# Kernel tuning notes

Hardware: AMD Instinct MI355X
Metric: run time of the kernel (lower is better)

The kernel has to match this reference:

```python
import jax, jax.numpy as jnp
import numpy as np

NEG_SLOPE = 0.2  # PyG GATConv default


def leaky_relu(v):
    return jnp.where(v >= 0, v, NEG_SLOPE * v)


def gat_conv(x, W, a_src, a_dst, b, src, dst, n_nodes):
    # x: [N, Fin], W: [Fin, Fout], a_src/a_dst/b: [Fout]
    h = x @ W                               # [N, Fout]
    alpha_src = h @ a_src                   # [N]
    alpha_dst = h @ a_dst                   # [N]
    e = leaky_relu(alpha_src[src] + alpha_dst[dst])          # [E]
    m = jax.ops.segment_max(e, dst, num_segments=n_nodes)    # [N] (self-loops => every node has >=1 edge)
    p = jnp.exp(e - m[dst])                                   # [E]
    s = jax.ops.segment_sum(p, dst, num_segments=n_nodes)     # [N]
    coef = p / s[dst]                                          # [E]
    out = jax.ops.segment_sum(coef[:, None] * h[src], dst, num_segments=n_nodes)
    return out + b


def setup_inputs() -> dict:
    key = jax.random.key(0)
    ks = jax.random.split(key, 20)
    N, E, DIN, DH, DOUT, G = 50000, 800000, 128, 256, 2, 512
    x = jax.random.normal(ks[0], (N, DIN), dtype=jnp.float32)
    edge_index = jax.random.randint(ks[1], (2, E), 0, N, dtype=jnp.int64)
    batch = jnp.sort(jax.random.randint(ks[2], (N,), 0, G, dtype=jnp.int64))

    def lin(k, fin, fout):
        return jax.random.normal(k, (fin, fout), dtype=jnp.float32) * (1.0 / np.sqrt(fin))

    def att(k, f):
        return jax.random.normal(k, (f,), dtype=jnp.float32) * (1.0 / np.sqrt(f))

    return {
        "x": x, "edge_index": edge_index, "batch": batch,
        "W1": lin(ks[3], DIN, DH), "as1": att(ks[4], DH), "ad1": att(ks[5], DH), "b1": jnp.zeros((DH,), jnp.float32),
        "W2": lin(ks[6], DH, DH),  "as2": att(ks[7], DH), "ad2": att(ks[8], DH), "b2": jnp.zeros((DH,), jnp.float32),
        "W3": lin(ks[9], DH, DH),  "as3": att(ks[10], DH), "ad3": att(ks[11], DH), "b3": jnp.zeros((DH,), jnp.float32),
        "Wfc": lin(ks[12], DH, DOUT), "bfc": jnp.zeros((DOUT,), jnp.float32),
    }


def reference(x, edge_index, batch, W1, as1, ad1, b1, W2, as2, ad2, b2, W3, as3, ad3, b3, Wfc, bfc):
    N = x.shape[0]
    G = 512  # number of graphs (static)
    # add self-loops (PyG GATConv default add_self_loops=True)
    loops = jnp.arange(N, dtype=edge_index.dtype)
    src = jnp.concatenate([edge_index[0], loops])
    dst = jnp.concatenate([edge_index[1], loops])

    h = jax.nn.relu(gat_conv(x, W1, as1, ad1, b1, src, dst, N))
    h = jax.nn.relu(gat_conv(h, W2, as2, ad2, b2, src, dst, N))
    h = jax.nn.relu(gat_conv(h, W3, as3, ad3, b3, src, dst, N))

    # global mean pool over graphs
    sums = jax.ops.segment_sum(h, batch, num_segments=G)                 # [G, DH]
    counts = jax.ops.segment_sum(jnp.ones((N,), h.dtype), batch, num_segments=G)
    pooled = sums / jnp.maximum(counts, 1.0)[:, None]

    logits = pooled @ Wfc + bfc                                           # [G, DOUT]
    return jax.nn.softmax(logits, axis=1)
```

## Files before the change

kernel.cpp:

```cpp
#include <hip/hip_runtime.h>
#include <hip/hip_bf16.h>

typedef short short8 __attribute__((ext_vector_type(8)));
typedef float floatx4 __attribute__((ext_vector_type(4)));
typedef unsigned short ushort_t;
typedef unsigned short ushort4v __attribute__((ext_vector_type(4)));

__device__ __forceinline__ ushort_t f2bf(float v) {
    __hip_bfloat16 h = __float2bfloat16(v);
    return *(ushort_t*)&h;
}
__device__ __forceinline__ float bf2f(ushort_t u) {
    return __uint_as_float(((unsigned)u) << 16);
}
__device__ __forceinline__ float4 ldh4(const ushort_t* p) {
    ushort4v u = *(const ushort4v*)p;
    return make_float4(bf2f(u.x), bf2f(u.y), bf2f(u.z), bf2f(u.w));
}


__device__ __forceinline__ void wsplit_store(const float* __restrict__ W, int K,
                                             ushort_t* __restrict__ Bthi,
                                             ushort_t* __restrict__ Btlo,
                                             int idx, bool permK) {
    int n = idx & 255, k = idx >> 8;
    int i = k & 63;
    int ko = permK ? ((k & ~63) | ((i & 3) << 4) | (i >> 2)) : k;
    float v = W[(size_t)ko * 256 + n];
    ushort_t h = f2bf(v);
    float r = v - bf2f(h);
    int nt = n >> 4, c = k >> 5, q = (k & 31) >> 3, j = k & 7;
    int l = q * 16 + (n & 15);
    size_t off = ((size_t)(nt * (K >> 5) + c) * 64 + l) * 8 + j;
    Bthi[off] = h;
    Btlo[off] = f2bf(r);
}

__global__ __launch_bounds__(256) void prep_kernel(const float* __restrict__ X,
                                                   ushort_t* __restrict__ Xhi,
                                                   ushort_t* __restrict__ Xlo,
                                                   int* __restrict__ deg,
                                                   float* __restrict__ asrcA,
                                                   float* __restrict__ adstA,
                                                   const float* __restrict__ W1,
                                                   const float* __restrict__ W2,
                                                   const float* __restrict__ W3,
                                                   ushort_t* __restrict__ B1h, ushort_t* __restrict__ B1l,
                                                   ushort_t* __restrict__ B2h, ushort_t* __restrict__ B2l,
                                                   ushort_t* __restrict__ B3h, ushort_t* __restrict__ B3l,
                                                   int total, int N) {
    int idx = blockIdx.x * 256 + threadIdx.x;
    if (idx < N) {
        deg[idx] = 0;
        asrcA[idx] = 0.f;
        adstA[idx] = 0.f;
    }
    const int S1 = 128 * 256, S2 = 256 * 256;
    if (idx < S1) {
        wsplit_store(W1, 128, B1h, B1l, idx, false);
    } else if (idx < S1 + S2) {
        wsplit_store(W2, 256, B2h, B2l, idx - S1, true);
    } else if (idx < S1 + 2 * S2) {
        wsplit_store(W3, 256, B3h, B3l, idx - S1 - S2, true);
    }
    if (idx < total) {
        float v = X[idx];
        ushort_t h = f2bf(v);
        Xhi[idx] = h;
        Xlo[idx] = f2bf(v - bf2f(h));
    }
}

template <int NCHUNK, bool HASLO>
__global__ __launch_bounds__(256) void gemm_mfma(const ushort_t* __restrict__ Ahi_g,
                                                 const ushort_t* __restrict__ Alo_g,
                                                 const ushort_t* __restrict__ Bthi,
                                                 const ushort_t* __restrict__ Btlo,
                                                 ushort_t* __restrict__ Hb,
                                                 const float* __restrict__ a_src,
                                                 const float* __restrict__ a_dst,
                                                 float* __restrict__ asrc_out,
                                                 float* __restrict__ adst_out,
                                                 int N) {
    constexpr int K = NCHUNK * 32;
    const int tid = threadIdx.x;
    const int wave = tid >> 6, lane = tid & 63;
    const int wr = wave & 1, wc = wave >> 1;
    const int q = lane >> 4, l15 = lane & 15;
    const int rowBase = blockIdx.x * 128;
    const int colBase = blockIdx.y * 128;

    floatx4 acc[4][4];
#pragma unroll
    for (int i = 0; i < 4; ++i)
#pragma unroll
        for (int j = 0; j < 4; ++j) acc[i][j] = (floatx4)0.f;

    size_t aoff[4];
#pragma unroll
    for (int mt = 0; mt < 4; ++mt) {
        int r = rowBase + wr * 64 + mt * 16 + l15;
        if (r > N - 1) r = N - 1;
        aoff[mt] = (size_t)r * K + q * 8;
    }

    const int ntg = blockIdx.y * 8 + wc * 4;
    const size_t ntstride = (size_t)NCHUNK * 512;
    const ushort_t* bhp = Bthi + (size_t)ntg * ntstride + (size_t)lane * 8;
    const ushort_t* blp = Btlo + (size_t)ntg * ntstride + (size_t)lane * 8;

#pragma unroll
    for (int c = 0; c < NCHUNK; ++c) {
        const int co = c * 32;
        const size_t cb = (size_t)c * 512;
        short8 ah[4], al[4], bh[4], bl[4];
#pragma unroll
        for (int mt = 0; mt < 4; ++mt)
            ah[mt] = *(const short8*)(Ahi_g + aoff[mt] + co);
        if (HASLO) {
#pragma unroll
            for (int mt = 0; mt < 4; ++mt)
                al[mt] = *(const short8*)(Alo_g + aoff[mt] + co);
        }
#pragma unroll
        for (int nt = 0; nt < 4; ++nt) {
            bh[nt] = *(const short8*)(bhp + (size_t)nt * ntstride + cb);
            bl[nt] = *(const short8*)(blp + (size_t)nt * ntstride + cb);
        }
#pragma unroll
        for (int mt = 0; mt < 4; ++mt)
#pragma unroll
            for (int nt = 0; nt < 4; ++nt) {
                acc[mt][nt] = __builtin_amdgcn_mfma_f32_16x16x32_bf16(ah[mt], bh[nt], acc[mt][nt], 0, 0, 0);
                acc[mt][nt] = __builtin_amdgcn_mfma_f32_16x16x32_bf16(ah[mt], bl[nt], acc[mt][nt], 0, 0, 0);
            }
        if (HASLO) {
#pragma unroll
            for (int mt = 0; mt < 4; ++mt)
#pragma unroll
                for (int nt = 0; nt < 4; ++nt)
                    acc[mt][nt] = __builtin_amdgcn_mfma_f32_16x16x32_bf16(al[mt], bh[nt], acc[mt][nt], 0, 0, 0);
        }
    }

    float asv[4], adv[4];
#pragma unroll
    for (int nt = 0; nt < 4; ++nt) {
        int n = colBase + wc * 64 + nt * 16 + l15;
        asv[nt] = a_src[n];
        adv[nt] = a_dst[n];
    }
#pragma unroll
    for (int mt = 0; mt < 4; ++mt) {
#pragma unroll
        for (int reg = 0; reg < 4; ++reg) {
            int grow = rowBase + wr * 64 + mt * 16 + q * 4 + reg;
            float p1 = acc[mt][0][reg] * asv[0] + acc[mt][1][reg] * asv[1] +
                       acc[mt][2][reg] * asv[2] + acc[mt][3][reg] * asv[3];
            float p2 = acc[mt][0][reg] * adv[0] + acc[mt][1][reg] * adv[1] +
                       acc[mt][2][reg] * adv[2] + acc[mt][3][reg] * adv[3];
            if (grow < N) {
                uint2 pk;
                pk.x = (unsigned)f2bf(acc[mt][0][reg]) | ((unsigned)f2bf(acc[mt][1][reg]) << 16);
                pk.y = (unsigned)f2bf(acc[mt][2][reg]) | ((unsigned)f2bf(acc[mt][3][reg]) << 16);
                *(uint2*)(Hb + (size_t)grow * 256 + colBase + wc * 64 + l15 * 4) = pk;
            }
#pragma unroll
            for (int off = 1; off < 16; off <<= 1) {
                p1 += __shfl_xor(p1, off, 64);
                p2 += __shfl_xor(p2, off, 64);
            }
            if (l15 == 0 && grow < N) {
                atomicAdd(&asrc_out[grow], p1);
                atomicAdd(&adst_out[grow], p2);
            }
        }
    }
}

__global__ __launch_bounds__(256) void count_kernel(const int* __restrict__ edst,
                                                    int* __restrict__ deg, int E) {
    int i = blockIdx.x * 256 + threadIdx.x;
    if (i < E) atomicAdd(&deg[edst[i]], 1);
}

__global__ __launch_bounds__(256) void scan1_kernel(const int* __restrict__ deg,
                                                    int* __restrict__ excl,
                                                    int* __restrict__ bsum, int N) {
    __shared__ int tmp[256];
    int tid = threadIdx.x;
    int i = blockIdx.x * 256 + tid;
    int v = (i < N) ? deg[i] : 0;
    tmp[tid] = v;
    __syncthreads();
    for (int off = 1; off < 256; off <<= 1) {
        int t = (tid >= off) ? tmp[tid - off] : 0;
        __syncthreads();
        tmp[tid] += t;
        __syncthreads();
    }
    if (i < N) excl[i] = tmp[tid] - v;
    if (tid == 255) bsum[blockIdx.x] = tmp[255];
}

__global__ __launch_bounds__(256) void scan2_kernel(int* __restrict__ bsum, int nb) {
    __shared__ int tmp[256];
    int tid = threadIdx.x;
    int v = (tid < nb) ? bsum[tid] : 0;
    tmp[tid] = v;
    __syncthreads();
    for (int off = 1; off < 256; off <<= 1) {
        int t = (tid >= off) ? tmp[tid - off] : 0;
        __syncthreads();
        tmp[tid] += t;
        __syncthreads();
    }
    if (tid < nb) bsum[tid] = tmp[tid] - v;
}

__global__ __launch_bounds__(256) void scan3_kernel(const int* __restrict__ excl,
                                                    const int* __restrict__ bsum,
                                                    int* __restrict__ rowptr,
                                                    int* __restrict__ cursor,
                                                    int N, int E) {
    int i = blockIdx.x * 256 + threadIdx.x;
    if (i < N) {
        int v = excl[i] + bsum[blockIdx.x];
        rowptr[i] = v;
        cursor[i] = v;
    }
    if (i == 0) rowptr[N] = E;
}

__global__ __launch_bounds__(256) void scatter_kernel(const int* __restrict__ esrc,
                                                      const int* __restrict__ edst,
                                                      int* __restrict__ cursor,
                                                      int* __restrict__ csr_src, int E) {
    int i = blockIdx.x * 256 + threadIdx.x;
    if (i < E) {
        int d = edst[i];
        int pos = atomicAdd(&cursor[d], 1);
        csr_src[pos] = esrc[i];
    }
}

__global__ __launch_bounds__(256) void gat_fused_kernel(const ushort_t* __restrict__ hb,
                                                        const float* __restrict__ asrc,
                                                        const float* __restrict__ adst,
                                                        const int* __restrict__ rowptr,
                                                        const int* __restrict__ csr_src,
                                                        const float* __restrict__ bias,
                                                        ushort_t* __restrict__ ohi,
                                                        float* __restrict__ asrc_next,
                                                        float* __restrict__ adst_next,
                                                        int N) {
    int wave = threadIdx.x >> 6;
    int lane = threadIdx.x & 63;
    int d = blockIdx.x * 4 + wave;
    if (d >= N) return;

    if (lane == 0) {
        asrc_next[d] = 0.f;
        adst_next[d] = 0.f;
    }

    const float* bb = bias + (lane >> 4) * 64 + (lane & 15);
    float b0 = bb[0], b1 = bb[16], b2 = bb[32], b3 = bb[48];

    float ad = adst[d];
    float es = asrc[d] + ad;
    es = es >= 0.f ? es : 0.2f * es;
    float m = es;
    float s = 1.0f;
    float4 acc = ldh4(hb + (size_t)d * 256 + lane * 4);

    int beg = rowptr[d], end = rowptr[d + 1];
    for (int base = beg; base < end; base += 64) {
        int cnt = min(64, end - base);
        int srci = 0;
        float e = -1e30f;
        if (lane < cnt) {
            srci = csr_src[base + lane];
            float v = asrc[srci] + ad;
            e = v >= 0.f ? v : 0.2f * v;
        }
        float cm = e;
#pragma unroll
        for (int off = 32; off > 0; off >>= 1) cm = fmaxf(cm, __shfl_xor(cm, off, 64));
        float mnew = fmaxf(m, cm);
        float scale = __expf(m - mnew);
        m = mnew;

        float p = __expf(e - m);
        float ps = p;
#pragma unroll
        for (int off = 32; off > 0; off >>= 1) ps += __shfl_xor(ps, off, 64);
        s = s * scale + ps;
        acc.x *= scale; acc.y *= scale; acc.z *= scale; acc.w *= scale;

        int j = 0;
        for (; j + 4 <= cnt; j += 4) {
            float p0 = __shfl(p, j, 64),     p1 = __shfl(p, j + 1, 64);
            float p2 = __shfl(p, j + 2, 64), p3 = __shfl(p, j + 3, 64);
            int s0 = __shfl(srci, j, 64),     s1i = __shfl(srci, j + 1, 64);
            int s2i = __shfl(srci, j + 2, 64), s3i = __shfl(srci, j + 3, 64);
            float4 hv0 = ldh4(hb + (size_t)s0 * 256 + lane * 4);
            float4 hv1 = ldh4(hb + (size_t)s1i * 256 + lane * 4);
            float4 hv2 = ldh4(hb + (size_t)s2i * 256 + lane * 4);
            float4 hv3 = ldh4(hb + (size_t)s3i * 256 + lane * 4);
            acc.x += p0 * hv0.x + p1 * hv1.x + p2 * hv2.x + p3 * hv3.x;
            acc.y += p0 * hv0.y + p1 * hv1.y + p2 * hv2.y + p3 * hv3.y;
            acc.z += p0 * hv0.z + p1 * hv1.z + p2 * hv2.z + p3 * hv3.z;
            acc.w += p0 * hv0.w + p1 * hv1.w + p2 * hv2.w + p3 * hv3.w;
        }
        for (; j < cnt; ++j) {
            float pj = __shfl(p, j, 64);
            int sj = __shfl(srci, j, 64);
            float4 hv = ldh4(hb + (size_t)sj * 256 + lane * 4);
            acc.x += pj * hv.x; acc.y += pj * hv.y; acc.z += pj * hv.z; acc.w += pj * hv.w;
        }
    }
    float inv = 1.0f / s;
    float ox = fmaxf(acc.x * inv + b0, 0.f);
    float oy = fmaxf(acc.y * inv + b1, 0.f);
    float oz = fmaxf(acc.z * inv + b2, 0.f);
    float ow = fmaxf(acc.w * inv + b3, 0.f);
    ushort4v hv;
    hv.x = f2bf(ox); hv.y = f2bf(oy); hv.z = f2bf(oz); hv.w = f2bf(ow);
    *(ushort4v*)(ohi + (size_t)d * 256 + lane * 4) = hv;
}

__device__ __forceinline__ int lower_bound_i(const int* __restrict__ a, int n, int v) {
    int lo = 0, hi = n;
    while (lo < hi) {
        int mid = (lo + hi) >> 1;
        if (a[mid] < v) lo = mid + 1; else hi = mid;
    }
    return lo;
}

__global__ __launch_bounds__(256) void pool_fc_kernel(const ushort_t* __restrict__ hhi,
                                                      const int* __restrict__ batch,
                                                      int N,
                                                      const float* __restrict__ Wfc,
                                                      const float* __restrict__ bfc,
                                                      float* __restrict__ out) {
    __shared__ float red0[256];
    __shared__ float red1[256];
    int g = blockIdx.x;
    int c = threadIdx.x;
    int i = c & 63;
    int o = (c & ~63) | ((i & 3) << 4) | (i >> 2);
    int beg = lower_bound_i(batch, N, g);
    int end = lower_bound_i(batch, N, g + 1);
    float sum = 0.f;
    for (int n = beg; n < end; ++n)
        sum += bf2f(hhi[(size_t)n * 256 + c]);
    float cnt = (float)(end - beg);
    float v = sum / fmaxf(cnt, 1.0f);
    red0[c] = v * Wfc[o * 2 + 0];
    red1[c] = v * Wfc[o * 2 + 1];
    __syncthreads();
    for (int off = 128; off > 0; off >>= 1) {
        if (c < off) {
            red0[c] += red0[c + off];
            red1[c] += red1[c + off];
        }
        __syncthreads();
    }
    if (c == 0) {
        float l0 = red0[0] + bfc[0];
        float l1 = red1[0] + bfc[1];
        float mx = fmaxf(l0, l1);
        float e0 = expf(l0 - mx), e1 = expf(l1 - mx);
        float s = e0 + e1;
        out[g * 2 + 0] = e0 / s;
        out[g * 2 + 1] = e1 / s;
    }
}

extern "C" void kernel_launch(void* const* d_in, const int* in_sizes, int n_in,
                              void* d_out, int out_size, void* d_ws, size_t ws_size,
                              hipStream_t stream) {
    const float* x    = (const float*)d_in[0];
    const int*   eidx = (const int*)d_in[1];
    const int*   batch= (const int*)d_in[2];
    const float* Wl[3]  = {(const float*)d_in[3], (const float*)d_in[7],  (const float*)d_in[11]};
    const float* asl[3] = {(const float*)d_in[4], (const float*)d_in[8],  (const float*)d_in[12]};
    const float* adl[3] = {(const float*)d_in[5], (const float*)d_in[9],  (const float*)d_in[13]};
    const float* bl[3]  = {(const float*)d_in[6], (const float*)d_in[10], (const float*)d_in[14]};
    const float* Wfc = (const float*)d_in[15];
    const float* bfc = (const float*)d_in[16];
    float* out = (float*)d_out;

    const int N   = in_sizes[2];
    const int E   = in_sizes[1] / 2;
    const int DIN = in_sizes[0] / N;
    const int DH  = 256;
    const int G   = 512;
    const int* esrc = eidx;
    const int* edst = eidx + E;

    char* ws = (char*)d_ws;
    size_t off = 0;
    const size_t featHalf = (size_t)N * DH * sizeof(ushort_t);
    ushort_t* hb     = (ushort_t*)(ws + off); off += featHalf;
    ushort_t* ghi    = (ushort_t*)(ws + off); off += featHalf;
    ushort_t* xhi    = (ushort_t*)(ws + off); off += (size_t)N * DIN * sizeof(ushort_t);
    ushort_t* xlo    = (ushort_t*)(ws + off); off += (size_t)N * DIN * sizeof(ushort_t);
    float*    asA    = (float*)(ws + off); off += (size_t)N * sizeof(float);
    float*    adA    = (float*)(ws + off); off += (size_t)N * sizeof(float);
    float*    asB    = (float*)(ws + off); off += (size_t)N * sizeof(float);
    float*    adB    = (float*)(ws + off); off += (size_t)N * sizeof(float);
    int*      deg    = (int*)(ws + off);   off += (size_t)N * sizeof(int);
    int*      excl   = (int*)(ws + off);   off += (size_t)N * sizeof(int);
    int*      rowptr = (int*)(ws + off);   off += (size_t)(N + 1) * sizeof(int);
    int*      cursor = (int*)(ws + off);   off += (size_t)N * sizeof(int);
    int*      bsum   = (int*)(ws + off);   off += 1024;
    int*      csrsrc = (int*)(ws + off);   off += (size_t)E * sizeof(int);
    ushort_t* B1h    = (ushort_t*)(ws + off); off += (size_t)128 * 256 * sizeof(ushort_t);
    ushort_t* B1l    = (ushort_t*)(ws + off); off += (size_t)128 * 256 * sizeof(ushort_t);
    ushort_t* B2h    = (ushort_t*)(ws + off); off += (size_t)256 * 256 * sizeof(ushort_t);
    ushort_t* B2l    = (ushort_t*)(ws + off); off += (size_t)256 * 256 * sizeof(ushort_t);
    ushort_t* B3h    = (ushort_t*)(ws + off); off += (size_t)256 * 256 * sizeof(ushort_t);
    ushort_t* B3l    = (ushort_t*)(ws + off); off += (size_t)256 * 256 * sizeof(ushort_t);

    const int nbN = (N + 255) / 256;

    prep_kernel<<<((size_t)N * DIN + 255) / 256, 256, 0, stream>>>(
        x, xhi, xlo, deg, asA, adA, Wl[0], Wl[1], Wl[2],
        B1h, B1l, B2h, B2l, B3h, B3l, N * DIN, N);

    count_kernel<<<(E + 255) / 256, 256, 0, stream>>>(edst, deg, E);
    scan1_kernel<<<nbN, 256, 0, stream>>>(deg, excl, bsum, N);
    scan2_kernel<<<1, 256, 0, stream>>>(bsum, nbN);
    scan3_kernel<<<nbN, 256, 0, stream>>>(excl, bsum, rowptr, cursor, N, E);
    scatter_kernel<<<(E + 255) / 256, 256, 0, stream>>>(esrc, edst, cursor, csrsrc, E);

    const ushort_t* Bh[3]  = {B1h, B2h, B3h};
    const ushort_t* Blp[3] = {B1l, B2l, B3l};
    float* asCur[3] = {asA, asB, asA};
    float* adCur[3] = {adA, adB, adA};
    float* asNext[3] = {asB, asA, asB};
    float* adNext[3] = {adB, adA, adB};

    dim3 ggrid((N + 127) / 128, 2);
    for (int layer = 0; layer < 3; ++layer) {
        if (layer == 0) {
            gemm_mfma<4, true><<<ggrid, 256, 0, stream>>>(xhi, xlo, Bh[0], Blp[0], hb,
                                                          asl[0], adl[0], asCur[0], adCur[0], N);
        } else {
            gemm_mfma<8, false><<<ggrid, 256, 0, stream>>>(ghi, nullptr, Bh[layer], Blp[layer], hb,
                                                           asl[layer], adl[layer],
                                                           asCur[layer], adCur[layer], N);
        }

        gat_fused_kernel<<<(N + 3) / 4, 256, 0, stream>>>(hb, asCur[layer], adCur[layer],
                                                          rowptr, csrsrc, bl[layer], ghi,
                                                          asNext[layer], adNext[layer], N);
    }

    pool_fc_kernel<<<G, 256, 0, stream>>>(ghi, batch, N, Wfc, bfc, out);
}
```

Measured before the change: 517.9 us.

## Give each GEMM wave full-width rows so attention scores need no atomics

The GEMM now launches one block per 128 rows instead of splitting columns across two blocks. Each wave computes 32 rows by all 256 columns, so the per-row attention dot products are complete inside the wave and are written with plain stores instead of atomicAdd. This removes the score zeroing in prep and gat kernels and the ping-pong buffers. The weight split in prep now writes coalesced. The trade-off is 128 accumulator registers per wave, which may lower occupancy, and B tiles are no longer reused across the wave's row tiles in the same way.

After: 610.4 us. 17.9% more time.

```diff
diff --git a/kernel.cpp b/kernel.cpp
--- a/kernel.cpp
+++ b/kernel.cpp
@@ -19,29 +19,30 @@
 }
 
 
-__device__ __forceinline__ void wsplit_store(const float* __restrict__ W, int K,
-                                             ushort_t* __restrict__ Bthi,
-                                             ushort_t* __restrict__ Btlo,
-                                             int idx, bool permK) {
-    int n = idx & 255, k = idx >> 8;
-    int i = k & 63;
-    int ko = permK ? ((k & ~63) | ((i & 3) << 4) | (i >> 2)) : k;
+template <int NCSHIFT>
+__device__ __forceinline__ void wsplit_coal(const float* __restrict__ W,
+                                            ushort_t* __restrict__ Bh,
+                                            ushort_t* __restrict__ Bl,
+                                            int o, bool permK) {
+    int j = o & 7;
+    int l = (o >> 3) & 63;
+    int rest = o >> 9;
+    int nt = rest >> NCSHIFT;
+    int c  = rest & ((1 << NCSHIFT) - 1);
+    int n  = nt * 16 + (l & 15);
+    int ks = c * 32 + (l >> 4) * 8 + j;
+    int i = ks & 63;
+    int ko = permK ? ((ks & ~63) | ((i & 3) << 4) | (i >> 2)) : ks;
     float v = W[(size_t)ko * 256 + n];
     ushort_t h = f2bf(v);
-    float r = v - bf2f(h);
-    int nt = n >> 4, c = k >> 5, q = (k & 31) >> 3, j = k & 7;
-    int l = q * 16 + (n & 15);
-    size_t off = ((size_t)(nt * (K >> 5) + c) * 64 + l) * 8 + j;
-    Bthi[off] = h;
-    Btlo[off] = f2bf(r);
+    Bh[o] = h;
+    Bl[o] = f2bf(v - bf2f(h));
 }
 
 __global__ __launch_bounds__(256) void prep_kernel(const float* __restrict__ X,
                                                    ushort_t* __restrict__ Xhi,
                                                    ushort_t* __restrict__ Xlo,
                                                    int* __restrict__ deg,
-                                                   float* __restrict__ asrcA,
-                                                   float* __restrict__ adstA,
                                                    const float* __restrict__ W1,
                                                    const float* __restrict__ W2,
                                                    const float* __restrict__ W3,
@@ -50,18 +51,14 @@
                                                    ushort_t* __restrict__ B3h, ushort_t* __restrict__ B3l,
                                                    int total, int N) {
     int idx = blockIdx.x * 256 + threadIdx.x;
-    if (idx < N) {
-        deg[idx] = 0;
-        asrcA[idx] = 0.f;
-        adstA[idx] = 0.f;
-    }
+    if (idx < N) deg[idx] = 0;
     const int S1 = 128 * 256, S2 = 256 * 256;
     if (idx < S1) {
-        wsplit_store(W1, 128, B1h, B1l, idx, false);
+        wsplit_coal<2>(W1, B1h, B1l, idx, false);
     } else if (idx < S1 + S2) {
-        wsplit_store(W2, 256, B2h, B2l, idx - S1, true);
+        wsplit_coal<3>(W2, B2h, B2l, idx - S1, true);
     } else if (idx < S1 + 2 * S2) {
-        wsplit_store(W3, 256, B3h, B3l, idx - S1 - S2, true);
+        wsplit_coal<3>(W3, B3h, B3l, idx - S1 - S2, true);
     }
     if (idx < total) {
         float v = X[idx];
@@ -85,85 +82,84 @@
     constexpr int K = NCHUNK * 32;
     const int tid = threadIdx.x;
     const int wave = tid >> 6, lane = tid & 63;
-    const int wr = wave & 1, wc = wave >> 1;
     const int q = lane >> 4, l15 = lane & 15;
-    const int rowBase = blockIdx.x * 128;
-    const int colBase = blockIdx.y * 128;
-
-    floatx4 acc[4][4];
-#pragma unroll
-    for (int i = 0; i < 4; ++i)
-#pragma unroll
-        for (int j = 0; j < 4; ++j) acc[i][j] = (floatx4)0.f;
-
-    size_t aoff[4];
-#pragma unroll
-    for (int mt = 0; mt < 4; ++mt) {
-        int r = rowBase + wr * 64 + mt * 16 + l15;
+    const int rowBase = blockIdx.x * 128 + wave * 32;
+
+    floatx4 acc[2][16];
+#pragma unroll
+    for (int i = 0; i < 2; ++i)
+#pragma unroll
+        for (int j = 0; j < 16; ++j) acc[i][j] = (floatx4)0.f;
+
+    size_t aoff[2];
+#pragma unroll
+    for (int mt = 0; mt < 2; ++mt) {
+        int r = rowBase + mt * 16 + l15;
         if (r > N - 1) r = N - 1;
         aoff[mt] = (size_t)r * K + q * 8;
     }
 
-    const int ntg = blockIdx.y * 8 + wc * 4;
     const size_t ntstride = (size_t)NCHUNK * 512;
-    const ushort_t* bhp = Bthi + (size_t)ntg * ntstride + (size_t)lane * 8;
-    const ushort_t* blp = Btlo + (size_t)ntg * ntstride + (size_t)lane * 8;
+    const ushort_t* bhp = Bthi + (size_t)lane * 8;
+    const ushort_t* blp = Btlo + (size_t)lane * 8;
 
 #pragma unroll
     for (int c = 0; c < NCHUNK; ++c) {
         const int co = c * 32;
         const size_t cb = (size_t)c * 512;
-        short8 ah[4], al[4], bh[4], bl[4];
-#pragma unroll
-        for (int mt = 0; mt < 4; ++mt)
+        short8 ah[2], al[2];
+#pragma unroll
+        for (int mt = 0; mt < 2; ++mt)
             ah[mt] = *(const short8*)(Ahi_g + aoff[mt] + co);
         if (HASLO) {
 #pragma unroll
-            for (int mt = 0; mt < 4; ++mt)
+            for (int mt = 0; mt < 2; ++mt)
                 al[mt] = *(const short8*)(Alo_g + aoff[mt] + co);
         }
 #pragma unroll
-        for (int nt = 0; nt < 4; ++nt) {
-            bh[nt] = *(const short8*)(bhp + (size_t)nt * ntstride + cb);
-            bl[nt] = *(const short8*)(blp + (size_t)nt * ntstride + cb);
-        }
-#pragma unroll
-        for (int mt = 0; mt < 4; ++mt)
-#pragma unroll
-            for (int nt = 0; nt < 4; ++nt) {
-                acc[mt][nt] = __builtin_amdgcn_mfma_f32_16x16x32_bf16(ah[mt], bh[nt], acc[mt][nt], 0, 0, 0);
-                acc[mt][nt] = __builtin_amdgcn_mfma_f32_16x16x32_bf16(ah[mt], bl[nt], acc[mt][nt], 0, 0, 0);
+        for (int nt = 0; nt < 16; ++nt) {
+            short8 bh = *(const short8*)(bhp + (size_t)nt * ntstride + cb);
+            short8 bl = *(const short8*)(blp + (size_t)nt * ntstride + cb);
+            acc[0][nt] = __builtin_amdgcn_mfma_f32_16x16x32_bf16(ah[0], bh, acc[0][nt], 0, 0, 0);
+            acc[0][nt] = __builtin_amdgcn_mfma_f32_16x16x32_bf16(ah[0], bl, acc[0][nt], 0, 0, 0);
+            acc[1][nt] = __builtin_amdgcn_mfma_f32_16x16x32_bf16(ah[1], bh, acc[1][nt], 0, 0, 0);
+            acc[1][nt] = __builtin_amdgcn_mfma_f32_16x16x32_bf16(ah[1], bl, acc[1][nt], 0, 0, 0);
+            if (HASLO) {
+                acc[0][nt] = __builtin_amdgcn_mfma_f32_16x16x32_bf16(al[0], bh, acc[0][nt], 0, 0, 0);
+                acc[1][nt] = __builtin_amdgcn_mfma_f32_16x16x32_bf16(al[1], bh, acc[1][nt], 0, 0, 0);
             }
-        if (HASLO) {
-#pragma unroll
-            for (int mt = 0; mt < 4; ++mt)
-#pragma unroll
-                for (int nt = 0; nt < 4; ++nt)
-                    acc[mt][nt] = __builtin_amdgcn_mfma_f32_16x16x32_bf16(al[mt], bh[nt], acc[mt][nt], 0, 0, 0);
-        }
-    }
-
-    float asv[4], adv[4];
-#pragma unroll
-    for (int nt = 0; nt < 4; ++nt) {
-        int n = colBase + wc * 64 + nt * 16 + l15;
+        }
+    }
+
+    float asv[16], adv[16];
+#pragma unroll
+    for (int nt = 0; nt < 16; ++nt) {
+        int n = nt * 16 + l15;
         asv[nt] = a_src[n];
         adv[nt] = a_dst[n];
     }
 #pragma unroll
-    for (int mt = 0; mt < 4; ++mt) {
+    for (int mt = 0; mt < 2; ++mt) {
 #pragma unroll
         for (int reg = 0; reg < 4; ++reg) {
-            int grow = rowBase + wr * 64 + mt * 16 + q * 4 + reg;
-            float p1 = acc[mt][0][reg] * asv[0] + acc[mt][1][reg] * asv[1] +
-                       acc[mt][2][reg] * asv[2] + acc[mt][3][reg] * asv[3];
-            float p2 = acc[mt][0][reg] * adv[0] + acc[mt][1][reg] * adv[1] +
-                       acc[mt][2][reg] * adv[2] + acc[mt][3][reg] * adv[3];
+            int grow = rowBase + mt * 16 + q * 4 + reg;
+            float p1 = 0.f, p2 = 0.f;
+#pragma unroll
+            for (int nt = 0; nt < 16; ++nt) {
+                p1 += acc[mt][nt][reg] * asv[nt];
+                p2 += acc[mt][nt][reg] * adv[nt];
+            }
             if (grow < N) {
-                uint2 pk;
-                pk.x = (unsigned)f2bf(acc[mt][0][reg]) | ((unsigned)f2bf(acc[mt][1][reg]) << 16);
-                pk.y = (unsigned)f2bf(acc[mt][2][reg]) | ((unsigned)f2bf(acc[mt][3][reg]) << 16);
-                *(uint2*)(Hb + (size_t)grow * 256 + colBase + wc * 64 + l15 * 4) = pk;
+                ushort_t* crow = Hb + (size_t)grow * 256 + l15 * 4;
+#pragma unroll
+                for (int g = 0; g < 4; ++g) {
+                    uint2 pk;
+                    pk.x = (unsigned)f2bf(acc[mt][4 * g + 0][reg]) |
+                           ((unsigned)f2bf(acc[mt][4 * g + 1][reg]) << 16);
+                    pk.y = (unsigned)f2bf(acc[mt][4 * g + 2][reg]) |
+                           ((unsigned)f2bf(acc[mt][4 * g + 3][reg]) << 16);
+                    *(uint2*)(crow + g * 64) = pk;
+                }
             }
 #pragma unroll
             for (int off = 1; off < 16; off <<= 1) {
@@ -171,8 +167,8 @@
                 p2 += __shfl_xor(p2, off, 64);
             }
             if (l15 == 0 && grow < N) {
-                atomicAdd(&asrc_out[grow], p1);
-                atomicAdd(&adst_out[grow], p2);
+                asrc_out[grow] = p1;
+                adst_out[grow] = p2;
             }
         }
     }
@@ -251,18 +247,11 @@
                                                         const int* __restrict__ csr_src,
                                                         const float* __restrict__ bias,
                                                         ushort_t* __restrict__ ohi,
-                                                        float* __restrict__ asrc_next,
-                                                        float* __restrict__ adst_next,
                                                         int N) {
     int wave = threadIdx.x >> 6;
     int lane = threadIdx.x & 63;
     int d = blockIdx.x * 4 + wave;
     if (d >= N) return;
-
-    if (lane == 0) {
-        asrc_next[d] = 0.f;
-        adst_next[d] = 0.f;
-    }
 
     const float* bb = bias + (lane >> 4) * 64 + (lane & 15);
     float b0 = bb[0], b1 = bb[16], b2 = bb[32], b3 = bb[48];
@@ -408,10 +397,8 @@
     ushort_t* ghi    = (ushort_t*)(ws + off); off += featHalf;
     ushort_t* xhi    = (ushort_t*)(ws + off); off += (size_t)N * DIN * sizeof(ushort_t);
     ushort_t* xlo    = (ushort_t*)(ws + off); off += (size_t)N * DIN * sizeof(ushort_t);
-    float*    asA    = (float*)(ws + off); off += (size_t)N * sizeof(float);
-    float*    adA    = (float*)(ws + off); off += (size_t)N * sizeof(float);
-    float*    asB    = (float*)(ws + off); off += (size_t)N * sizeof(float);
-    float*    adB    = (float*)(ws + off); off += (size_t)N * sizeof(float);
+    float*    asrc   = (float*)(ws + off); off += (size_t)N * sizeof(float);
+    float*    adst   = (float*)(ws + off); off += (size_t)N * sizeof(float);
     int*      deg    = (int*)(ws + off);   off += (size_t)N * sizeof(int);
     int*      excl   = (int*)(ws + off);   off += (size_t)N * sizeof(int);
     int*      rowptr = (int*)(ws + off);   off += (size_t)(N + 1) * sizeof(int);
@@ -428,7 +415,7 @@
     const int nbN = (N + 255) / 256;
 
     prep_kernel<<<((size_t)N * DIN + 255) / 256, 256, 0, stream>>>(
-        x, xhi, xlo, deg, asA, adA, Wl[0], Wl[1], Wl[2],
+        x, xhi, xlo, deg, Wl[0], Wl[1], Wl[2],
         B1h, B1l, B2h, B2l, B3h, B3l, N * DIN, N);
 
     count_kernel<<<(E + 255) / 256, 256, 0, stream>>>(edst, deg, E);
@@ -439,25 +426,20 @@
 
     const ushort_t* Bh[3]  = {B1h, B2h, B3h};
     const ushort_t* Blp[3] = {B1l, B2l, B3l};
-    float* asCur[3] = {asA, asB, asA};
-    float* adCur[3] = {adA, adB, adA};
-    float* asNext[3] = {asB, asA, asB};
-    float* adNext[3] = {adB, adA, adB};
-
-    dim3 ggrid((N + 127) / 128, 2);
+
+    dim3 ggrid((N + 127) / 128);
     for (int layer = 0; layer < 3; ++layer) {
         if (layer == 0) {
             gemm_mfma<4, true><<<ggrid, 256, 0, stream>>>(xhi, xlo, Bh[0], Blp[0], hb,
-                                                          asl[0], adl[0], asCur[0], adCur[0], N);
+                                                          asl[0], adl[0], asrc, adst, N);
         } else {
             gemm_mfma<8, false><<<ggrid, 256, 0, stream>>>(ghi, nullptr, Bh[layer], Blp[layer], hb,
                                                            asl[layer], adl[layer],
-                                                           asCur[layer], adCur[layer], N);
-        }
-
-        gat_fused_kernel<<<(N + 3) / 4, 256, 0, stream>>>(hb, asCur[layer], adCur[layer],
-                                                          rowptr, csrsrc, bl[layer], ghi,
-                                                          asNext[layer], adNext[layer], N);
+                                                           asrc, adst, N);
+        }
+
+        gat_fused_kernel<<<(N + 3) / 4, 256, 0, stream>>>(hb, asrc, adst,
+                                                          rowptr, csrsrc, bl[layer], ghi, N);
     }
 
     pool_fc_kernel<<<G, 256, 0, stream>>>(ghi, batch, N, Wfc, bfc, out);
```
